# Performance work log

Measured on AMD Instinct MI355X. Metric: run time of the kernel, lower is better.

The kernel has to match this reference:

```python
import jax, jax.numpy as jnp
import numpy as np

B, T, U = 4, 250, 120
EPROJS, DUNITS, EMBED, JOINT, ODIM, ATT = 512, 512, 512, 512, 1024, 512
BLANK = 0


def _p(key, shape, scale=0.02):
    return jax.random.normal(key, shape, dtype=jnp.float32) * scale


def setup_inputs() -> dict:
    key = jax.random.key(0)
    ks = jax.random.split(key, 24)
    hs_pad = jax.random.normal(ks[0], (B, T, EPROJS), dtype=jnp.float32)
    ys_in_pad = jax.random.randint(ks[1], (B, U), 0, ODIM)
    hlens = jax.random.randint(ks[2], (B,), T // 2, T + 1).astype(jnp.int32)
    embed = _p(ks[3], (ODIM, EMBED)).at[BLANK].set(0.0)  # padding_idx=blank
    # LSTMCell layer 0: input = embed + eprojs
    W_ih0 = _p(ks[4], (4 * DUNITS, EMBED + EPROJS)); b_ih0 = jnp.zeros((4 * DUNITS,), jnp.float32)
    W_hh0 = _p(ks[5], (4 * DUNITS, DUNITS));          b_hh0 = jnp.zeros((4 * DUNITS,), jnp.float32)
    # LSTMCell layer 1
    W_ih1 = _p(ks[6], (4 * DUNITS, DUNITS)); b_ih1 = jnp.zeros((4 * DUNITS,), jnp.float32)
    W_hh1 = _p(ks[7], (4 * DUNITS, DUNITS)); b_hh1 = jnp.zeros((4 * DUNITS,), jnp.float32)
    # additive attention (AttAdd): mlp_enc (bias), mlp_dec (no bias), gvec
    W_att_enc = _p(ks[8], (EPROJS, ATT)); b_att_enc = jnp.zeros((ATT,), jnp.float32)
    W_att_dec = _p(ks[9], (DUNITS, ATT))
    gvec = _p(ks[10], (ATT,))
    # joint network
    W_lin_enc = _p(ks[11], (JOINT, EPROJS)); b_lin_enc = jnp.zeros((JOINT,), jnp.float32)
    W_lin_dec = _p(ks[12], (JOINT, DUNITS))  # bias=False
    W_lin_out = _p(ks[13], (ODIM, JOINT));   b_lin_out = jnp.zeros((ODIM,), jnp.float32)
    return dict(hs_pad=hs_pad, ys_in_pad=ys_in_pad, hlens=hlens, embed=embed,
                W_ih0=W_ih0, b_ih0=b_ih0, W_hh0=W_hh0, b_hh0=b_hh0,
                W_ih1=W_ih1, b_ih1=b_ih1, W_hh1=W_hh1, b_hh1=b_hh1,
                W_att_enc=W_att_enc, b_att_enc=b_att_enc, W_att_dec=W_att_dec, gvec=gvec,
                W_lin_enc=W_lin_enc, b_lin_enc=b_lin_enc, W_lin_dec=W_lin_dec,
                W_lin_out=W_lin_out, b_lin_out=b_lin_out)


def _lstm_cell(x, h, c, W_ih, b_ih, W_hh, b_hh):
    g = x @ W_ih.T + b_ih + h @ W_hh.T + b_hh
    i, f, gg, o = jnp.split(g, 4, axis=-1)  # torch gate order: i, f, g, o
    c_new = jax.nn.sigmoid(f) * c + jax.nn.sigmoid(i) * jnp.tanh(gg)
    h_new = jax.nn.sigmoid(o) * jnp.tanh(c_new)
    return h_new, c_new


def reference(hs_pad, ys_in_pad, hlens, embed,
              W_ih0, b_ih0, W_hh0, b_hh0, W_ih1, b_ih1, W_hh1, b_hh1,
              W_att_enc, b_att_enc, W_att_dec, gvec,
              W_lin_enc, b_lin_enc, W_lin_dec, W_lin_out, b_lin_out):
    Bq, Tq = hs_pad.shape[0], hs_pad.shape[1]
    eys = embed[ys_in_pad]  # (B, U, E)
    pre_enc = hs_pad @ W_att_enc + b_att_enc  # (B, T, A), computed once
    mask = jnp.arange(Tq)[None, :] < hlens[:, None]  # (B, T)

    def step(carry, ey_i):
        z0, c0, z1, c1 = carry
        # additive attention: scores over encoder frames
        q = z0 @ W_att_dec  # (B, A)
        e = jnp.tanh(pre_enc + q[:, None, :]) @ gvec  # (B, T)
        e = jnp.where(mask, e, -1e9)
        w = jax.nn.softmax(e, axis=-1)
        att_c = jnp.einsum('bt,btd->bd', w, hs_pad)  # (B, eprojs)
        ey = jnp.concatenate([ey_i, att_c], axis=1)  # (B, E+eprojs)
        z0n, c0n = _lstm_cell(ey, z0, c0, W_ih0, b_ih0, W_hh0, b_hh0)
        z1n, c1n = _lstm_cell(z0n, z1, c1, W_ih1, b_ih1, W_hh1, b_hh1)
        return (z0n, c0n, z1n, c1n), z1n

    zeros = jnp.zeros((Bq, DUNITS), hs_pad.dtype)
    _, ys = jax.lax.scan(step, (zeros, zeros, zeros, zeros),
                         jnp.swapaxes(eys, 0, 1))  # ys: (U, B, D)
    h_dec = jnp.swapaxes(ys, 0, 1)  # (B, U, D)

    # joint: broadcast add of enc/dec projections, tanh, output proj
    henc = hs_pad @ W_lin_enc.T + b_lin_enc  # (B, T, J)
    hdec = h_dec @ W_lin_dec.T               # (B, U, J)
    z = jnp.tanh(henc[:, :, None, :] + hdec[:, None, :, :])  # (B, T, U, J)
    return z @ W_lin_out.T + b_lin_out  # (B, T, U, odim)
```

## Files before the change

### kernel.cpp

```cpp
#include <hip/hip_runtime.h>

#define B_ 4
#define T_ 250
#define U_ 120
#define D_ 512
#define G_ 2048
#define O_ 1024
#define NBLK 256

typedef __attribute__((ext_vector_type(8))) short bf16x8;
typedef __attribute__((ext_vector_type(4))) float f32x4;
typedef __attribute__((ext_vector_type(4))) unsigned int ui4;

__device__ __forceinline__ float tanh_fast(float x){
  float e = __expf(2.f*x);
  return 1.f - 2.f/(e + 1.f);
}
__device__ __forceinline__ float sigmoid_fast(float x){
  return 1.f/(1.f + __expf(-x));
}
__device__ __forceinline__ unsigned short f2bf(float x){
  unsigned int u = __float_as_uint(x);
  unsigned int r = (u + 0x7FFFu + ((u >> 16) & 1u)) >> 16;
  return (unsigned short)r;
}

__device__ __forceinline__ void atomStoreF(float* p, float v){
  __hip_atomic_store(p, v, __ATOMIC_RELAXED, __HIP_MEMORY_SCOPE_AGENT);
}
__device__ __forceinline__ void mall_load4f(const float* p0, const float* p1,
    const float* p2, const float* p3, float& v0, float& v1, float& v2, float& v3){
  asm volatile(
    "global_load_dword %0, %4, off sc0 sc1\n\t"
    "global_load_dword %1, %5, off sc0 sc1\n\t"
    "global_load_dword %2, %6, off sc0 sc1\n\t"
    "global_load_dword %3, %7, off sc0 sc1\n\t"
    "s_waitcnt vmcnt(0)"
    : "=&v"(v0), "=&v"(v1), "=&v"(v2), "=&v"(v3)
    : "v"(p0), "v"(p1), "v"(p2), "v"(p3)
    : "memory");
}

__device__ __forceinline__ void gbar_arrive(int* flags, int gen){
  __syncthreads();
  if (threadIdx.x == 0){
    asm volatile("s_waitcnt vmcnt(0)" ::: "memory");
    __hip_atomic_store(&flags[blockIdx.x*16], gen, __ATOMIC_RELAXED,
                       __HIP_MEMORY_SCOPE_AGENT);
  }
}
__device__ __forceinline__ void gbar_wait(int* flags, int* rel, int gen){
  if (blockIdx.x == 0){
    if (threadIdx.x < 64){
      int l = threadIdx.x;
      const int* p0 = flags + (l*4+0)*16;
      const int* p1 = flags + (l*4+1)*16;
      const int* p2 = flags + (l*4+2)*16;
      const int* p3 = flags + (l*4+3)*16;
      long c = 0;
      while (true){
        int f0,f1,f2,f3;
        asm volatile(
          "global_load_dword %0, %4, off sc0 sc1\n\t"
          "global_load_dword %1, %5, off sc0 sc1\n\t"
          "global_load_dword %2, %6, off sc0 sc1\n\t"
          "global_load_dword %3, %7, off sc0 sc1\n\t"
          "s_waitcnt vmcnt(0)"
          : "=&v"(f0),"=&v"(f1),"=&v"(f2),"=&v"(f3)
          : "v"(p0), "v"(p1), "v"(p2), "v"(p3)
          : "memory");
        int m0 = f0 < f1 ? f0 : f1;
        int m1 = f2 < f3 ? f2 : f3;
        int mm = m0 < m1 ? m0 : m1;
        if (__all(mm >= gen)) break;
        if (++c > (1L<<22)) break;
      }
      if (threadIdx.x == 0)
        __hip_atomic_store(rel, gen, __ATOMIC_RELAXED,
                           __HIP_MEMORY_SCOPE_AGENT);
    }
  } else {
    if (threadIdx.x == 0){
      long c = 0;
      while (__hip_atomic_load(rel, __ATOMIC_RELAXED,
                               __HIP_MEMORY_SCOPE_AGENT) < gen){
        if (++c > (1L<<22)) break;
      }
    }
  }
  __syncthreads();
}
__device__ __forceinline__ void gbar(int* flags, int* rel, int gen){
  gbar_arrive(flags, gen);
  gbar_wait(flags, rel, gen);
}

__global__ void barinit_k(int* flags){
  int i = blockIdx.x*256 + threadIdx.x;
  if (i < NBLK*16 + 16)
    __hip_atomic_store(&flags[i], 0, __ATOMIC_RELAXED, __HIP_MEMORY_SCOPE_AGENT);
}

__global__ void gather_embed_k(const int* __restrict__ ys, const float* __restrict__ embed,
                               float* __restrict__ eys){
  int i = blockIdx.x*256 + threadIdx.x;
  if (i < B_*U_*D_){
    int r = i >> 9, k = i & 511;
    eys[i] = embed[ys[r]*D_ + k];
  }
}

__device__ __forceinline__ void gemm64_nt_body(float* smem,
  const float* __restrict__ A, int lda, const float* __restrict__ B, int ldb,
  const float* __restrict__ bias, float* __restrict__ C, int ldc,
  int M, int N, int K, int bx, int by)
{
  float (*As)[65] = (float(*)[65])smem;
  float (*Bs)[65] = (float(*)[65])(smem + 16*65);
  int tid = threadIdx.x;
  int m0 = by*64, n0 = bx*64;
  int tx = tid & 15, ty = tid >> 4;
  float acc[4][4] = {};
  for (int k0 = 0; k0 < K; k0 += 16){
#pragma unroll
    for (int i=0;i<4;i++){
      int e = tid + 256*i;
      int mm = e >> 4, kk = e & 15;
      int mg = m0 + mm;
      As[kk][mm] = (mg < M) ? A[(size_t)mg*lda + k0 + kk] : 0.f;
      int ng = n0 + mm;
      Bs[kk][mm] = (ng < N) ? B[(size_t)ng*ldb + k0 + kk] : 0.f;
    }
    __syncthreads();
#pragma unroll
    for (int kk=0;kk<16;kk++){
      float av[4], bv[4];
#pragma unroll
      for (int i=0;i<4;i++) av[i] = As[kk][ty*4+i];
#pragma unroll
      for (int j=0;j<4;j++) bv[j] = Bs[kk][tx*4+j];
#pragma unroll
      for (int i=0;i<4;i++)
#pragma unroll
        for (int j=0;j<4;j++) acc[i][j] += av[i]*bv[j];
    }
    __syncthreads();
  }
#pragma unroll
  for (int i=0;i<4;i++){
    int m = m0 + ty*4 + i;
    if (m < M){
#pragma unroll
      for (int j=0;j<4;j++){
        int n = n0 + tx*4 + j;
        if (n < N) C[(size_t)m*ldc + n] = acc[i][j] + (bias ? bias[n] : 0.f);
      }
    }
  }
}

__device__ __forceinline__ void gemm64_nn_body(float* smem,
  const float* __restrict__ A, int lda, const float* __restrict__ B, int ldb,
  const float* __restrict__ bias, float* __restrict__ C, int ldc,
  int M, int N, int K, int bx, int by)
{
  float (*As)[65] = (float(*)[65])smem;
  float (*Bs)[65] = (float(*)[65])(smem + 16*65);
  int tid = threadIdx.x;
  int m0 = by*64, n0 = bx*64;
  int tx = tid & 15, ty = tid >> 4;
  float acc[4][4] = {};
  for (int k0 = 0; k0 < K; k0 += 16){
#pragma unroll
    for (int i=0;i<4;i++){
      int e = tid + 256*i;
      int mm = e >> 4, kk = e & 15;
      int mg = m0 + mm;
      As[kk][mm] = (mg < M) ? A[(size_t)mg*lda + k0 + kk] : 0.f;
      int nn = e & 63, kk2 = e >> 6;
      int ng = n0 + nn;
      Bs[kk2][nn] = (ng < N) ? B[(size_t)(k0+kk2)*ldb + ng] : 0.f;
    }
    __syncthreads();
#pragma unroll
    for (int kk=0;kk<16;kk++){
      float av[4], bv[4];
#pragma unroll
      for (int i=0;i<4;i++) av[i] = As[kk][ty*4+i];
#pragma unroll
      for (int j=0;j<4;j++) bv[j] = Bs[kk][tx*4+j];
#pragma unroll
      for (int i=0;i<4;i++)
#pragma unroll
        for (int j=0;j<4;j++) acc[i][j] += av[i]*bv[j];
    }
    __syncthreads();
  }
#pragma unroll
  for (int i=0;i<4;i++){
    int m = m0 + ty*4 + i;
    if (m < M){
#pragma unroll
      for (int j=0;j<4;j++){
        int n = n0 + tx*4 + j;
        if (n < N) C[(size_t)m*ldc + n] = acc[i][j] + (bias ? bias[n] : 0.f);
      }
    }
  }
}

__global__ __launch_bounds__(256) void pre_gemms_k(
  const float* __restrict__ hs, const float* __restrict__ eys,
  const float* __restrict__ W_att_enc, const float* __restrict__ b_att_enc,
  const float* __restrict__ W_lin_enc, const float* __restrict__ b_lin_enc,
  const float* __restrict__ W_ih0,
  float* __restrict__ pre_enc, float* __restrict__ henc,
  float* __restrict__ pre0, float* __restrict__ hsW0)
{
  __shared__ float smem[2*16*65];
  int id = blockIdx.x;
  if (id < 128){
    gemm64_nn_body(smem, hs,512, W_att_enc,512, b_att_enc, pre_enc,512,
                   B_*T_,512,512, id & 7, id >> 3);
  } else if (id < 256){
    id -= 128;
    gemm64_nt_body(smem, hs,512, W_lin_enc,512, b_lin_enc, henc,512,
                   B_*T_,512,512, id & 7, id >> 3);
  } else if (id < 512){
    id -= 256;
    gemm64_nt_body(smem, eys,512, W_ih0,1024, nullptr, pre0,2048,
                   B_*U_,2048,512, id & 31, id >> 5);
  } else {
    id -= 512;
    gemm64_nt_body(smem, hs,512, W_ih0+512,1024, nullptr, hsW0,2048,
                   B_*T_,2048,512, id & 31, id >> 5);
  }
}

__global__ __launch_bounds__(256) void gemm64_nt_k(
  const float* __restrict__ A, int lda, const float* __restrict__ B, int ldb,
  const float* __restrict__ bias, float* __restrict__ C, int ldc,
  int M, int N, int K)
{
  __shared__ float smem[2*16*65];
  gemm64_nt_body(smem, A,lda,B,ldb,bias,C,ldc,M,N,K, blockIdx.x, blockIdx.y);
}

__global__ __launch_bounds__(256) void scan_k(
    float* __restrict__ z0, float* __restrict__ z1,
    float* __restrict__ q,  float* __restrict__ e,
    int* __restrict__ flags, int* __restrict__ rel,
    const float* __restrict__ pre_enc, const float* __restrict__ pre0,
    const float* __restrict__ hsW0,
    const float* __restrict__ W_hh0, const float* __restrict__ W_ih1,
    const float* __restrict__ W_hh1, const float* __restrict__ W_att_dec,
    const float* __restrict__ gvec, const int* __restrict__ hlens,
    const float* __restrict__ b_ih0, const float* __restrict__ b_hh0,
    const float* __restrict__ b_ih1, const float* __restrict__ b_hh1,
    float* __restrict__ h_dec)
{
  int bk = blockIdx.x, tid = threadIdx.x;
  int lane = tid & 63, wv = tid >> 6;
  int d0 = bk * 2;

  __shared__ float whh0_s[8*512];
  __shared__ float whh1_s[8*512];
  __shared__ float wih1_s[8*512];
  __shared__ float wdec_s[2*512];
  __shared__ float hsw_s[4*8*256];
  __shared__ float pre0_s[480*8];
  __shared__ float pre_s[4*512];
  __shared__ float gvec_s[512];
  __shared__ float zs0[2048], zs1[2048], qs[2048];
  __shared__ float pA0[32], pA1[32], gB[32], gC[32];
  __shared__ float bias0_s[8], bias1_s[8], c0_s[8], c1_s[8];
  __shared__ int hlens_s[4];

  for (int idx = tid; idx < 8*512; idx += 256){
    int gd = idx >> 9, k = idx & 511;
    int j = (gd >> 1)*512 + d0 + (gd & 1);
    whh0_s[idx] = W_hh0[(size_t)j*512 + k];
    whh1_s[idx] = W_hh1[(size_t)j*512 + k];
    wih1_s[idx] = W_ih1[(size_t)j*512 + k];
  }
  for (int idx = tid; idx < 2*512; idx += 256){
    int dd = idx >> 9, k = idx & 511;
    wdec_s[idx] = W_att_dec[(size_t)k*512 + d0 + dd];
  }
  for (int idx = tid; idx < 4*1000; idx += 256){
    int gp = idx & 3, tg = idx >> 2;
    int b = tg / 250, t = tg - b*250;
    const float2 v = *(const float2*)(hsW0 + (size_t)tg*G_ + gp*512 + d0);
    hsw_s[(b*8 + gp*2 + 0)*256 + t] = v.x;
    hsw_s[(b*8 + gp*2 + 1)*256 + t] = v.y;
  }
  for (int idx = tid; idx < 4*8*6; idx += 256){
    int t = 250 + (idx % 6), bg = idx / 6;
    hsw_s[bg*256 + t] = 0.f;
  }
  for (int idx = tid; idx < 480*4; idx += 256){
    int gp = idx & 3, r = idx >> 2;
    const float2 v = *(const float2*)(pre0 + (size_t)r*G_ + gp*512 + d0);
    pre0_s[r*8 + gp*2 + 0] = v.x;
    pre0_s[r*8 + gp*2 + 1] = v.y;
  }
  for (int idx = tid; idx < 4*512; idx += 256){
    int r = bk*4 + (idx >> 9);
    pre_s[idx] = (r < B_*T_) ? pre_enc[(size_t)r*512 + (idx & 511)] : 0.f;
  }
  for (int idx = tid; idx < 512; idx += 256) gvec_s[idx] = gvec[idx];
  for (int idx = tid; idx < 2048; idx += 256) zs0[idx] = 0.f;
  if (tid < 4) hlens_s[tid] = hlens[tid];
  if (tid < 32){ pA0[tid] = 0.f; }
  if (tid < 8){
    int j = ((tid >> 1))*512 + d0 + (tid & 1);
    bias0_s[tid] = b_ih0[j] + b_hh0[j];
    bias1_s[tid] = b_ih1[j] + b_hh1[j];
    c0_s[tid] = 0.f; c1_s[tid] = 0.f;
    int b = tid >> 1, d = d0 + (tid & 1);
    atomStoreF(&z1[b*512 + d], 0.f);
    atomStoreF(&q [b*512 + d], 0.f);
  }
  int gen = 0;
  gbar(flags, rel, ++gen);

  for (int u = 0; u < U_; ++u){
    {
      float vz[8], vq[8];
#pragma unroll
      for (int i=0;i<8;i++)
        asm volatile("global_load_dword %0, %1, off sc0 sc1"
                     : "=&v"(vz[i]) : "v"(&z1[tid + 256*i]));
#pragma unroll
      for (int i=0;i<8;i++)
        asm volatile("global_load_dword %0, %1, off sc0 sc1"
                     : "=&v"(vq[i]) : "v"(&q[tid + 256*i]));
      asm volatile("s_waitcnt vmcnt(0)" ::: "memory");
#pragma unroll
      for (int i=0;i<8;i++){ zs1[tid + 256*i] = vz[i]; qs[tid + 256*i] = vq[i]; }
    }
    __syncthreads();
    {
      int r = bk*4 + wv;
      if (r < B_*T_){
        int b = r / 250, t = r - b*250;
        float s = 0.f;
#pragma unroll
        for (int i=0;i<8;i++){
          int k = i*64 + lane;
          float x = pre_s[wv*512+k] + qs[b*512+k];
          s += tanh_fast(x) * gvec_s[k];
        }
#pragma unroll
        for (int off=32; off; off>>=1) s += __shfl_xor(s, off);
        if (lane == 0) atomStoreF(&e[r], (t < hlens_s[b]) ? s : -1e30f);
      }
    }
    gbar_arrive(flags, ++gen);
    {
      int gd0 = wv*2, gd1 = wv*2 + 1;
      float a10[4]={}, a11[4]={};
#pragma unroll
      for (int i = 0; i < 8; ++i){
        int k = i*64 + lane;
        float w10 = whh1_s[gd0*512+k], w11 = whh1_s[gd1*512+k];
#pragma unroll
        for (int b=0;b<4;b++){
          float zv1 = zs1[b*512+k];
          a10[b] += w10*zv1; a11[b] += w11*zv1;
        }
      }
#pragma unroll
      for (int b=0;b<4;b++){
#pragma unroll
        for (int off=32; off; off>>=1){
          a10[b] += __shfl_xor(a10[b],off); a11[b] += __shfl_xor(a11[b],off);
        }
      }
      if (lane == 0){
#pragma unroll
        for (int b=0;b<4;b++){ pA1[b*8+gd0] = a10[b]; pA1[b*8+gd1] = a11[b]; }
      }
    }
    gbar_wait(flags, rel, gen);
    {
      int b = wv;
      const float* eb = e + b*250;
      float vals[4], w_reg[4];
      int t3 = 192 + lane;
      mall_load4f(eb + lane, eb + 64 + lane, eb + 128 + lane,
                  eb + (t3 < 250 ? t3 : 249),
                  vals[0], vals[1], vals[2], vals[3]);
      if (t3 >= 250) vals[3] = -1e30f;
      float vmax = fmaxf(fmaxf(vals[0],vals[1]), fmaxf(vals[2],vals[3]));
#pragma unroll
      for (int off=32; off; off>>=1) vmax = fmaxf(vmax, __shfl_xor(vmax, off));
      float ssum = 0.f;
#pragma unroll
      for (int i=0;i<4;i++){
        int t = i*64 + lane;
        w_reg[i] = (t < 250) ? __expf(vals[i] - vmax) : 0.f;
        ssum += w_reg[i];
      }
#pragma unroll
      for (int off=32; off; off>>=1) ssum += __shfl_xor(ssum, off);
      float inv = 1.f / ssum;
#pragma unroll
      for (int i=0;i<4;i++) w_reg[i] *= inv;

      float ag[8] = {};
#pragma unroll
      for (int i=0;i<4;i++){
        int t = i*64 + lane;
#pragma unroll
        for (int gd=0; gd<8; gd++)
          ag[gd] += w_reg[i] * hsw_s[(b*8+gd)*256 + t];
      }
#pragma unroll
      for (int gd=0; gd<8; gd++){
#pragma unroll
        for (int off=32; off; off>>=1) ag[gd] += __shfl_xor(ag[gd], off);
      }
      if (lane == 0){
#pragma unroll
        for (int gd=0; gd<8; gd++)
          gB[b*8+gd] = ag[gd] + pA0[b*8+gd] + pre0_s[(b*U_+u)*8 + gd] + bias0_s[gd];
      }
    }
    __syncthreads();
    if (tid < 8){
      int b = tid >> 1, dd = tid & 1;
      float ig = sigmoid_fast(gB[b*8 + 0 + dd]);
      float fg = sigmoid_fast(gB[b*8 + 2 + dd]);
      float gg = tanh_fast  (gB[b*8 + 4 + dd]);
      float og = sigmoid_fast(gB[b*8 + 6 + dd]);
      float cn = fg * c0_s[tid] + ig * gg;
      c0_s[tid] = cn;
      atomStoreF(&z0[b*512 + d0 + dd], og * tanh_fast(cn));
    }
    gbar(flags, rel, ++gen);
    {
      float vza[8];
#pragma unroll
      for (int i=0;i<8;i++)
        asm volatile("global_load_dword %0, %1, off sc0 sc1"
                     : "=&v"(vza[i]) : "v"(&z0[tid + 256*i]));
      asm volatile("s_waitcnt vmcnt(0)" ::: "memory");
#pragma unroll
      for (int i=0;i<8;i++) zs0[tid + 256*i] = vza[i];
    }
    __syncthreads();
    {
      int gd0 = wv*2, gd1 = wv*2 + 1;
      float a0[4]={}, a1[4]={};
#pragma unroll
      for (int i=0;i<8;i++){
        int k = i*64 + lane;
        float w0 = wih1_s[gd0*512+k], w1 = wih1_s[gd1*512+k];
#pragma unroll
        for (int b=0;b<4;b++){
          float zv = zs0[b*512+k];
          a0[b] += w0*zv; a1[b] += w1*zv;
        }
      }
#pragma unroll
      for (int b=0;b<4;b++){
#pragma unroll
        for (int off=32; off; off>>=1){
          a0[b] += __shfl_xor(a0[b],off); a1[b] += __shfl_xor(a1[b],off);
        }
      }
      if (lane == 0){
#pragma unroll
        for (int b=0;b<4;b++){
          gC[b*8+gd0] = a0[b] + pA1[b*8+gd0] + bias1_s[gd0];
          gC[b*8+gd1] = a1[b] + pA1[b*8+gd1] + bias1_s[gd1];
        }
      }
      if (wv < 2){
        float qa[4] = {};
#pragma unroll
        for (int i=0;i<8;i++){
          int k = i*64 + lane;
          float wq = wdec_s[wv*512+k];
#pragma unroll
          for (int b=0;b<4;b++) qa[b] += wq * zs0[b*512+k];
        }
#pragma unroll
        for (int b=0;b<4;b++){
#pragma unroll
          for (int off=32; off; off>>=1) qa[b] += __shfl_xor(qa[b],off);
        }
        if (lane == 0){
#pragma unroll
          for (int b=0;b<4;b++) atomStoreF(&q[b*512 + d0 + wv], qa[b]);
        }
      }
    }
    __syncthreads();
    if (tid < 8){
      int b = tid >> 1, dd = tid & 1;
      float ig = sigmoid_fast(gC[b*8 + 0 + dd]);
      float fg = sigmoid_fast(gC[b*8 + 2 + dd]);
      float gg = tanh_fast  (gC[b*8 + 4 + dd]);
      float og = sigmoid_fast(gC[b*8 + 6 + dd]);
      float cn = fg * c1_s[tid] + ig * gg;
      c1_s[tid] = cn;
      float hn = og * tanh_fast(cn);
      atomStoreF(&z1[b*512 + d0 + dd], hn);
      h_dec[((size_t)(b*U_ + u))*512 + d0 + dd] = hn;
    }
    gbar_arrive(flags, ++gen);
    {
      int gd0 = wv*2, gd1 = wv*2 + 1;
      float a00[4]={}, a01[4]={};
#pragma unroll
      for (int i = 0; i < 8; ++i){
        int k = i*64 + lane;
        float w00 = whh0_s[gd0*512+k], w01 = whh0_s[gd1*512+k];
#pragma unroll
        for (int b=0;b<4;b++){
          float zv0 = zs0[b*512+k];
          a00[b] += w00*zv0; a01[b] += w01*zv0;
        }
      }
#pragma unroll
      for (int b=0;b<4;b++){
#pragma unroll
        for (int off=32; off; off>>=1){
          a00[b] += __shfl_xor(a00[b],off); a01[b] += __shfl_xor(a01[b],off);
        }
      }
      if (lane == 0){
#pragma unroll
        for (int b=0;b<4;b++){ pA0[b*8+gd0] = a00[b]; pA0[b*8+gd1] = a01[b]; }
      }
    }
    gbar_wait(flags, rel, gen);
  }
}

__global__ __launch_bounds__(256) void pack_k(
    const float* __restrict__ henc, const float* __restrict__ hdec,
    unsigned short* __restrict__ P,
    const float* __restrict__ Wlin, unsigned short* __restrict__ Wb)
{
  const int NP8 = B_*T_*U_*512/8;
  int i = blockIdx.x*256 + threadIdx.x;
  if (i < NP8){
    int e = i*8;
    int k = e & 511;
    int r = e >> 9;
    int u = r % U_;
    int bt = r / U_;
    int b = bt / T_;
    const float* hp = henc + (size_t)bt*512 + k;
    const float* dp = hdec + (size_t)(b*U_ + u)*512 + k;
    unsigned int w[4];
#pragma unroll
    for (int j=0;j<4;j++){
      unsigned short lo = f2bf(tanh_fast(hp[2*j]   + dp[2*j]));
      unsigned short hi = f2bf(tanh_fast(hp[2*j+1] + dp[2*j+1]));
      w[j] = (unsigned int)lo | ((unsigned int)hi << 16);
    }
    *(ui4*)(P + e) = ui4{w[0], w[1], w[2], w[3]};
  } else {
    int j8 = i - NP8;
    if (j8 < O_*512/8){
      int e = j8*8;
      unsigned int w[4];
#pragma unroll
      for (int j=0;j<4;j++){
        unsigned short lo = f2bf(Wlin[e+2*j]);
        unsigned short hi = f2bf(Wlin[e+2*j+1]);
        w[j] = (unsigned int)lo | ((unsigned int)hi << 16);
      }
      *(ui4*)(Wb + e) = ui4{w[0], w[1], w[2], w[3]};
    }
  }
}

__global__ __launch_bounds__(256) void joint_mfma_k(
    const unsigned short* __restrict__ P,
    const unsigned short* __restrict__ Wb,
    const float* __restrict__ bout,
    float* __restrict__ out)
{
  __shared__ __align__(16) char smraw[32768];
  unsigned short* As = (unsigned short*)smraw;
  unsigned short* Bs = (unsigned short*)(smraw + 16384);
  float* outb = (float*)smraw;
  int tid = threadIdx.x;
  int lane = tid & 63;
  int w = tid >> 6, wr = w >> 1, wc = w & 1;
  int id = blockIdx.x;
  int bt = id % 1000;
  int ot = id / 1000;
  int o0 = ot * 128;
  const char* Pbase = (const char*)(P + (size_t)bt*U_*512);
  const char* Wbase = (const char*)(Wb + (size_t)o0*512);

  f32x4 acc[4][4] = {};

  for (int k0 = 0; k0 < 512; k0 += 64){
    __syncthreads();
#pragma unroll
    for (int j=0;j<4;j++){
      int pos = (j*256 + tid)*16;
      int row = pos >> 7;
      int inrow = pos & 127;
      int srcin = inrow ^ ((row & 7) << 4);
      int arow = row < U_ ? row : (U_-1);
      __builtin_amdgcn_global_load_lds(
        (const __attribute__((address_space(1))) void*)(Pbase + (size_t)arow*1024 + k0*2 + srcin),
        (__attribute__((address_space(3))) void*)((char*)As + pos), 16, 0, 0);
      __builtin_amdgcn_global_load_lds(
        (const __attribute__((address_space(1))) void*)(Wbase + (size_t)row*1024 + k0*2 + srcin),
        (__attribute__((address_space(3))) void*)((char*)Bs + pos), 16, 0, 0);
    }
    __syncthreads();
#pragma unroll
    for (int kk=0; kk<2; kk++){
      bf16x8 a[4], bb[4];
#pragma unroll
      for (int m=0;m<4;m++){
        int row = wr*64 + m*16 + (lane & 15);
        int inrow = (kk*64 + (lane >> 4)*16) ^ ((row & 7) << 4);
        a[m] = *(const bf16x8*)((const char*)As + row*128 + inrow);
      }
#pragma unroll
      for (int n=0;n<4;n++){
        int row = wc*64 + n*16 + (lane & 15);
        int inrow = (kk*64 + (lane >> 4)*16) ^ ((row & 7) << 4);
        bb[n] = *(const bf16x8*)((const char*)Bs + row*128 + inrow);
      }
#pragma unroll
      for (int m=0;m<4;m++)
#pragma unroll
        for (int n=0;n<4;n++)
          acc[m][n] = __builtin_amdgcn_mfma_f32_16x16x32_bf16(a[m], bb[n], acc[m][n], 0, 0, 0);
    }
  }
  float bv[4];
#pragma unroll
  for (int n=0;n<4;n++) bv[n] = bout[o0 + wc*64 + n*16 + (lane & 15)];
#pragma unroll
  for (int m=0;m<4;m++){
    __syncthreads();
#pragma unroll
    for (int n=0;n<4;n++){
      int col = wc*64 + n*16 + (lane & 15);
      int r0 = wr*16 + ((lane >> 4) << 2);
#pragma unroll
      for (int r=0;r<4;r++)
        outb[(r0+r)*132 + col] = acc[m][n][r] + bv[n];
    }
    __syncthreads();
    int row = tid >> 3;
    int c0  = (tid & 7) * 16;
    int u = (row < 16) ? (m*16 + row) : (64 + m*16 + (row - 16));
    if (u < U_){
      float* op = out + ((size_t)bt*U_ + u)*O_ + o0 + c0;
      const float* sp = &outb[row*132 + c0];
#pragma unroll
      for (int i=0;i<4;i++) *(f32x4*)(op + 4*i) = *(const f32x4*)(sp + 4*i);
    }
  }
}

extern "C" void kernel_launch(void* const* d_in, const int* in_sizes, int n_in,
                              void* d_out, int out_size, void* d_ws, size_t ws_size,
                              hipStream_t stream) {
  const float* hs       = (const float*)d_in[0];
  const int*   ys       = (const int*)  d_in[1];
  const int*   hlens    = (const int*)  d_in[2];
  const float* embed    = (const float*)d_in[3];
  const float* W_ih0    = (const float*)d_in[4];
  const float* b_ih0    = (const float*)d_in[5];
  const float* W_hh0    = (const float*)d_in[6];
  const float* b_hh0    = (const float*)d_in[7];
  const float* W_ih1    = (const float*)d_in[8];
  const float* b_ih1    = (const float*)d_in[9];
  const float* W_hh1    = (const float*)d_in[10];
  const float* b_hh1    = (const float*)d_in[11];
  const float* W_att_enc= (const float*)d_in[12];
  const float* b_att_enc= (const float*)d_in[13];
  const float* W_att_dec= (const float*)d_in[14];
  const float* gvec     = (const float*)d_in[15];
  const float* W_lin_enc= (const float*)d_in[16];
  const float* b_lin_enc= (const float*)d_in[17];
  const float* W_lin_dec= (const float*)d_in[18];
  const float* W_lin_out= (const float*)d_in[19];
  const float* b_lin_out= (const float*)d_in[20];
  float* out = (float*)d_out;

  float* w = (float*)d_ws;
  float* z0      = w;
  float* z1      = w + 2048;
  float* q       = w + 4096;
  float* e       = w + 6144;
  int*   flags   = (int*)(w + 7168);
  int*   rel     = flags + NBLK*16;
  float* eys     = w + 11776;
  float* pre_enc = w + 257536;
  float* pre0    = w + 769536;
  float* henc    = w + 1752576;
  float* h_dec   = w + 2264576;
  float* hdec_p  = w + 2510336;
  float* hsW0    = w + 2756096;
  unsigned short* Pbf = (unsigned short*)(w + 4804096);
  unsigned short* Wbf = (unsigned short*)(w + 4804096 + 30720000);

  barinit_k<<<17, 256, 0, stream>>>(flags);
  gather_embed_k<<<(B_*U_*D_ + 255)/256, 256, 0, stream>>>(ys, embed, eys);
  pre_gemms_k<<<1024, 256, 0, stream>>>(hs, eys, W_att_enc, b_att_enc,
                                        W_lin_enc, b_lin_enc, W_ih0,
                                        pre_enc, henc, pre0, hsW0);

  {
    void* args[] = {
      (void*)&z0, (void*)&z1, (void*)&q, (void*)&e, (void*)&flags, (void*)&rel,
      (void*)&pre_enc, (void*)&pre0, (void*)&hsW0,
      (void*)&W_hh0, (void*)&W_ih1, (void*)&W_hh1, (void*)&W_att_dec,
      (void*)&gvec, (void*)&hlens,
      (void*)&b_ih0, (void*)&b_hh0, (void*)&b_ih1, (void*)&b_hh1,
      (void*)&h_dec
    };
    hipLaunchCooperativeKernel((const void*)scan_k, dim3(NBLK), dim3(256),
                               args, 0, stream);
  }

  gemm64_nt_k<<<dim3(8, 8), 256, 0, stream>>>(h_dec, 512, W_lin_dec, 512, nullptr,
                                              hdec_p, 512, B_*U_, 512, 512);
  {
    const int NP8 = B_*T_*U_*512/8;
    const int NW8 = O_*512/8;
    pack_k<<<(NP8 + NW8 + 255)/256, 256, 0, stream>>>(henc, hdec_p, Pbf,
                                                      W_lin_out, Wbf);
  }
  joint_mfma_k<<<8000, 256, 0, stream>>>(Pbf, Wbf, b_lin_out, out);
}
```

Measured before the change: 1.909 ms.

## Double-buffer joint MFMA GEMM LDS loads and fold barrier init into gather

```diff
diff --git a/kernel.cpp b/kernel.cpp
--- a/kernel.cpp
+++ b/kernel.cpp
@@ -95,15 +95,11 @@
   gbar_wait(flags, rel, gen);
 }
 
-__global__ void barinit_k(int* flags){
+__global__ void gather_embed_k(const int* __restrict__ ys, const float* __restrict__ embed,
+                               float* __restrict__ eys, int* __restrict__ flags){
   int i = blockIdx.x*256 + threadIdx.x;
   if (i < NBLK*16 + 16)
     __hip_atomic_store(&flags[i], 0, __ATOMIC_RELAXED, __HIP_MEMORY_SCOPE_AGENT);
-}
-
-__global__ void gather_embed_k(const int* __restrict__ ys, const float* __restrict__ embed,
-                               float* __restrict__ eys){
-  int i = blockIdx.x*256 + threadIdx.x;
   if (i < B_*U_*D_){
     int r = i >> 9, k = i & 511;
     eys[i] = embed[ys[r]*D_ + k];
@@ -586,9 +582,7 @@
     const float* __restrict__ bout,
     float* __restrict__ out)
 {
-  __shared__ __align__(16) char smraw[32768];
-  unsigned short* As = (unsigned short*)smraw;
-  unsigned short* Bs = (unsigned short*)(smraw + 16384);
+  __shared__ __align__(16) char smraw[65536];
   float* outb = (float*)smraw;
   int tid = threadIdx.x;
   int lane = tid & 63;
@@ -602,23 +596,31 @@
 
   f32x4 acc[4][4] = {};
 
-  for (int k0 = 0; k0 < 512; k0 += 64){
-    __syncthreads();
-#pragma unroll
-    for (int j=0;j<4;j++){
-      int pos = (j*256 + tid)*16;
-      int row = pos >> 7;
-      int inrow = pos & 127;
-      int srcin = inrow ^ ((row & 7) << 4);
-      int arow = row < U_ ? row : (U_-1);
-      __builtin_amdgcn_global_load_lds(
-        (const __attribute__((address_space(1))) void*)(Pbase + (size_t)arow*1024 + k0*2 + srcin),
-        (__attribute__((address_space(3))) void*)((char*)As + pos), 16, 0, 0);
-      __builtin_amdgcn_global_load_lds(
-        (const __attribute__((address_space(1))) void*)(Wbase + (size_t)row*1024 + k0*2 + srcin),
-        (__attribute__((address_space(3))) void*)((char*)Bs + pos), 16, 0, 0);
-    }
-    __syncthreads();
+#define JSTAGE(bufofs, k0q) \
+  { _Pragma("unroll") \
+    for (int j=0;j<4;j++){ \
+      int pos = (j*256 + tid)*16; \
+      int row = pos >> 7; \
+      int inrow = pos & 127; \
+      int srcin = inrow ^ ((row & 7) << 4); \
+      int arow = row < U_ ? row : (U_-1); \
+      __builtin_amdgcn_global_load_lds( \
+        (const __attribute__((address_space(1))) void*)(Pbase + (size_t)arow*1024 + (k0q)*2 + srcin), \
+        (__attribute__((address_space(3))) void*)(smraw + (bufofs) + pos), 16, 0, 0); \
+      __builtin_amdgcn_global_load_lds( \
+        (const __attribute__((address_space(1))) void*)(Wbase + (size_t)row*1024 + (k0q)*2 + srcin), \
+        (__attribute__((address_space(3))) void*)(smraw + (bufofs) + 16384 + pos), 16, 0, 0); \
+    } }
+
+  int cur = 0;
+  JSTAGE(0, 0);
+  asm volatile("s_waitcnt vmcnt(0)" ::: "memory");
+  __syncthreads();
+#pragma unroll
+  for (int t = 0; t < 8; ++t){
+    if (t < 7) JSTAGE(cur ^ 32768, (t+1)*64);
+    const char* As = smraw + cur;
+    const char* Bs = smraw + cur + 16384;
 #pragma unroll
     for (int kk=0; kk<2; kk++){
       bf16x8 a[4], bb[4];
@@ -626,13 +628,13 @@
       for (int m=0;m<4;m++){
         int row = wr*64 + m*16 + (lane & 15);
         int inrow = (kk*64 + (lane >> 4)*16) ^ ((row & 7) << 4);
-        a[m] = *(const bf16x8*)((const char*)As + row*128 + inrow);
+        a[m] = *(const bf16x8*)(As + row*128 + inrow);
       }
 #pragma unroll
       for (int n=0;n<4;n++){
         int row = wc*64 + n*16 + (lane & 15);
         int inrow = (kk*64 + (lane >> 4)*16) ^ ((row & 7) << 4);
-        bb[n] = *(const bf16x8*)((const char*)Bs + row*128 + inrow);
+        bb[n] = *(const bf16x8*)(Bs + row*128 + inrow);
       }
 #pragma unroll
       for (int m=0;m<4;m++)
@@ -640,7 +642,12 @@
         for (int n=0;n<4;n++)
           acc[m][n] = __builtin_amdgcn_mfma_f32_16x16x32_bf16(a[m], bb[n], acc[m][n], 0, 0, 0);
     }
-  }
+    asm volatile("s_waitcnt vmcnt(0)" ::: "memory");
+    __syncthreads();
+    cur ^= 32768;
+  }
+#undef JSTAGE
+
   float bv[4];
 #pragma unroll
   for (int n=0;n<4;n++) bv[n] = bout[o0 + wc*64 + n*16 + (lane & 15)];
@@ -711,8 +718,7 @@
   unsigned short* Pbf = (unsigned short*)(w + 4804096);
   unsigned short* Wbf = (unsigned short*)(w + 4804096 + 30720000);
 
-  barinit_k<<<17, 256, 0, stream>>>(flags);
-  gather_embed_k<<<(B_*U_*D_ + 255)/256, 256, 0, stream>>>(ys, embed, eys);
+  gather_embed_k<<<(B_*U_*D_ + 255)/256, 256, 0, stream>>>(ys, embed, eys, flags);
   pre_gemms_k<<<1024, 256, 0, stream>>>(hs, eys, W_att_enc, b_att_enc,
                                         W_lin_enc, b_lin_enc, W_ih0,
                                         pre_enc, henc, pre0, hsW0);
```

New measurement: 1.900 ms. Within noise of the previous version (-0.5%).
